# Kernel optimization log

Measured on AMD Instinct MI355X. Metric: run time of the kernel, lower is better.

Reference implementation:

```python
import jax, jax.numpy as jnp
import numpy as np

B = 512          # graphs
M = 200          # nodes per graph
N = B * M        # 102400 total nodes
E = N * 32       # 3,276,800 edges
DIM_IN = 128
K = 30           # SortPool k
F = 32 + 32 + 32 + 1  # concat feature dim = 97


def setup_inputs() -> dict:
    key = jax.random.key(0)
    ks = jax.random.split(key, 20)
    x = jax.random.normal(ks[0], (N, DIM_IN), jnp.float32)
    # within-graph random edges so that batched SortPool is meaningful
    eg = jnp.repeat(jnp.arange(B, dtype=jnp.int32), E // B)  # graph id per edge
    src = eg * M + jax.random.randint(ks[1], (E,), 0, M, dtype=jnp.int32)
    dst = eg * M + jax.random.randint(ks[2], (E,), 0, M, dtype=jnp.int32)
    edge_index = jnp.stack([src, dst])  # [2, E]
    batch = jnp.arange(N, dtype=jnp.int32) // M  # sorted graph assignment

    def lin(k, fi, fo):
        s = 1.0 / np.sqrt(fi)
        return jax.random.uniform(k, (fi, fo), jnp.float32, -s, s)

    inp = {
        "x": x, "edge_index": edge_index, "batch": batch,
        "W1": lin(ks[3], DIM_IN, 32), "b1": jnp.zeros((32,), jnp.float32),
        "W2": lin(ks[4], 32, 32), "b2": jnp.zeros((32,), jnp.float32),
        "W3": lin(ks[5], 32, 32), "b3": jnp.zeros((32,), jnp.float32),
        "W4": lin(ks[6], 32, 1),  "b4": jnp.zeros((1,), jnp.float32),
        "convW1": jax.random.normal(ks[7], (16, 1, 97), jnp.float32) * 0.05,
        "convb1": jnp.zeros((16,), jnp.float32),
        "convW2": jax.random.normal(ks[8], (32, 16, 5), jnp.float32) * 0.05,
        "convb2": jnp.zeros((32,), jnp.float32),
        "linW1": lin(ks[9], 352, 128), "linb1": jnp.zeros((128,), jnp.float32),
        "linW2": lin(ks[10], 128, 1),  "linb2": jnp.zeros((1,), jnp.float32),
    }
    return inp


def _gcn(x, W, b, src, dst, dinv):
    """PyG GCNConv: D^-1/2 (A+I) D^-1/2 X W + b (degrees include self-loops)."""
    xw = x @ W                                   # [N, Fout]
    norm = dinv[src] * dinv[dst]                 # [E]
    agg = jax.ops.segment_sum(xw[src] * norm[:, None], dst, num_segments=N)
    agg = agg + xw * (dinv * dinv)[:, None]      # self-loop term
    return agg + b


def reference(x, edge_index, batch, W1, b1, W2, b2, W3, b3, W4, b4,
              convW1, convb1, convW2, convb2, linW1, linb1, linW2, linb2):
    src, dst = edge_index[0], edge_index[1]
    deg = jax.ops.segment_sum(jnp.ones((E,), x.dtype), dst, num_segments=N) + 1.0
    dinv = jax.lax.rsqrt(deg)

    h1 = jnp.tanh(_gcn(x, W1, b1, src, dst, dinv))
    h2 = jnp.tanh(_gcn(h1, W2, b2, src, dst, dinv))
    h3 = jnp.tanh(_gcn(h2, W3, b3, src, dst, dinv))
    h4 = jnp.tanh(_gcn(h3, W4, b4, src, dst, dinv))
    h = jnp.concatenate([h1, h2, h3, h4], axis=-1)  # [N, 97]

    # SortPool: batch is block-contiguous with M nodes/graph -> dense [B, M, F]
    hd = h.reshape(B, M, F)
    order = jnp.argsort(-hd[:, :, -1], axis=1)[:, :K]          # top-K by last channel
    top = jnp.take_along_axis(hd, order[:, :, None], axis=1)   # [B, K, 97]

    seq = top.reshape(B, 1, K * F)                             # [B, 1, 2910]
    dn = ("NCH", "OIH", "NCH")
    c1 = jax.lax.conv_general_dilated(seq, convW1, (97,), "VALID",
                                      dimension_numbers=dn) + convb1[None, :, None]
    c1 = jax.nn.relu(c1)                                       # [B, 16, 30]
    c1 = c1.reshape(B, 16, 15, 2).max(axis=-1)                 # MaxPool1d(2,2)
    c2 = jax.lax.conv_general_dilated(c1, convW2, (1,), "VALID",
                                      dimension_numbers=dn) + convb2[None, :, None]
    c2 = jax.nn.relu(c2)                                       # [B, 32, 11]

    flat = c2.reshape(B, 352)
    hlin = jax.nn.relu(flat @ linW1 + linb1)                   # dropout = identity (eval)
    out = jax.nn.sigmoid(hlin @ linW2 + linb2)                 # [B, 1]
    return out
```

## Files before the change

### kernel.cpp

```cpp
#include <hip/hip_runtime.h>
#include <hip/hip_fp16.h>


#define TPB   512
#define GRID  512
#define MG    200
#define EPG   6400
#define EE    (512 * EPG)

#define OFF_BUFX 0
#define OFF_HCUR 28944
#define OFF_CSR  57744
#define OFF_ROFF 64944
#define OFF_CNT  65760
#define OFF_CUR  66560
#define OFF_DINV 67360
#define OFF_H4   68160
#define OFF_RANK 68960
#define OFF_ORD  69760
#define OFF_BIAS 69880
#define OFF_RED  70136
#define OFF_WREG 70208
#define OFF_HIST 74560
#define OFF_PERM 74688
#define SMEM_BYTES 75488

#define QPAD 0xC8C8C8C8u

__device__ __forceinline__ float fast_tanh(float x) {
    const float e = __expf(2.0f * x);
    return 1.0f - 2.0f / (e + 1.0f);
}

__global__ __launch_bounds__(TPB)
void dgcnn_kernel(
    const float* __restrict__ x,
    const int*   __restrict__ ei,
    const float* __restrict__ W1, const float* __restrict__ b1,
    const float* __restrict__ W2, const float* __restrict__ b2,
    const float* __restrict__ W3, const float* __restrict__ b3,
    const float* __restrict__ W4, const float* __restrict__ b4,
    const float* __restrict__ cW1, const float* __restrict__ cb1,
    const float* __restrict__ cW2, const float* __restrict__ cb2,
    const float* __restrict__ lW1, const float* __restrict__ lb1,
    const float* __restrict__ lW2, const float* __restrict__ lb2,
    __half* __restrict__ arch,
    float* __restrict__ out)
{
    extern __shared__ unsigned char smem[];
    float* bufX = (float*)(smem + OFF_BUFX);
    float* hcur = (float*)(smem + OFF_HCUR);
    unsigned char* csr = (unsigned char*)(smem + OFF_CSR);
    int*   roff = (int*)(smem + OFF_ROFF);
    int*   cnt  = (int*)(smem + OFF_CNT);
    int*   cur  = (int*)(smem + OFF_CUR);
    float* dinv = (float*)(smem + OFF_DINV);
    float* h4k  = (float*)(smem + OFF_H4);
    int*   rank = (int*)(smem + OFF_RANK);
    int*   ord  = (int*)(smem + OFF_ORD);
    float* bias = (float*)(smem + OFF_BIAS);
    float* red  = (float*)(smem + OFF_RED);
    float* wreg = (float*)(smem + OFF_WREG);
    int*   hist = (int*)(smem + OFF_HIST);
    int*   perm = (int*)(smem + OFF_PERM);

    const int g = blockIdx.x;
    const int t = threadIdx.x;
    const int gbase = g * MG;
    const float* xg   = x + (size_t)gbase * 128;
    const int*   srcp = ei + (size_t)g * EPG;
    const int*   dstp = ei + (size_t)EE + (size_t)g * EPG;

    for (int idx = t; idx < 4096; idx += TPB)
        hcur[(idx & 31) * 132 + (idx >> 5)] = W1[idx];
    for (int idx = t; idx < 1800; idx += TPB)
        ((unsigned*)csr)[idx] = QPAD;
    if (t < 32) bias[t] = b1[t];
    if (t < MG) { cnt[t] = 0; rank[t] = 0; }
    if (t >= 480) hist[t - 480] = 0;
    if (t >= 256 && t < 292) bufX[200 * 36 + (t - 256)] = 0.f;
    __syncthreads();

    const int f32lane = t & 31;
    const int islot   = t >> 5;

    {
        const int4* d4p = (const int4*)dstp;
        for (int e4 = t; e4 < EPG / 4; e4 += TPB) {
            const int4 d4 = d4p[e4];
            atomicAdd(&cnt[d4.x - gbase], 1);
            atomicAdd(&cnt[d4.y - gbase], 1);
            atomicAdd(&cnt[d4.z - gbase], 1);
            atomicAdd(&cnt[d4.w - gbase], 1);
        }
    }
    {
        const int f = f32lane;
        const float* wt = hcur + f * 132;
        const float4* xv = (const float4*)xg;
        #pragma unroll
        for (int j0 = 0; j0 < 12; j0 += 6) {
            const int r0 = islot + 16 * j0;
            float a0 = 0.f, a1 = 0.f, a2 = 0.f, a3 = 0.f, a4 = 0.f, a5 = 0.f;
            #pragma unroll 2
            for (int k4 = 0; k4 < 32; ++k4) {
                const float4 w = *(const float4*)(wt + 4 * k4);
                float4 v;
                v = xv[(r0      ) * 32 + k4]; a0 += v.x*w.x + v.y*w.y + v.z*w.z + v.w*w.w;
                v = xv[(r0 + 16 ) * 32 + k4]; a1 += v.x*w.x + v.y*w.y + v.z*w.z + v.w*w.w;
                v = xv[(r0 + 32 ) * 32 + k4]; a2 += v.x*w.x + v.y*w.y + v.z*w.z + v.w*w.w;
                v = xv[(r0 + 48 ) * 32 + k4]; a3 += v.x*w.x + v.y*w.y + v.z*w.z + v.w*w.w;
                v = xv[(r0 + 64 ) * 32 + k4]; a4 += v.x*w.x + v.y*w.y + v.z*w.z + v.w*w.w;
                v = xv[(r0 + 80 ) * 32 + k4]; a5 += v.x*w.x + v.y*w.y + v.z*w.z + v.w*w.w;
            }
            bufX[(r0      ) * 36 + f] = a0;
            bufX[(r0 + 16 ) * 36 + f] = a1;
            bufX[(r0 + 32 ) * 36 + f] = a2;
            bufX[(r0 + 48 ) * 36 + f] = a3;
            bufX[(r0 + 64 ) * 36 + f] = a4;
            bufX[(r0 + 80 ) * 36 + f] = a5;
        }
        if (islot < 8) {
            const int r = 192 + islot;
            float a0 = 0.f;
            #pragma unroll 2
            for (int k4 = 0; k4 < 32; ++k4) {
                const float4 w = *(const float4*)(wt + 4 * k4);
                const float4 v = xv[r * 32 + k4];
                a0 += v.x*w.x + v.y*w.y + v.z*w.z + v.w*w.w;
            }
            bufX[r * 36 + f] = a0;
        }
    }
    __syncthreads();

    if (t >= 256 && t < 256 + MG) {
        const int i = t - 256;
        const int c = cnt[i];
        dinv[i] = 1.0f / sqrtf((float)(c + 1));
        int qc = (c + 4) >> 2;
        if (qc > 31) qc = 31;
        atomicAdd(&hist[31 - qc], 1);
    }
    if (t < 64) {
        if (t == 0) roff[0] = 0;
        int carry = 0;
        #pragma unroll
        for (int c = 0; c < 4; ++c) {
            const int i = c * 64 + t;
            int v = (i < MG) ? ((cnt[i] + 4) & ~3) : 0;
            #pragma unroll
            for (int off = 1; off < 64; off <<= 1) {
                int u = __shfl_up(v, off);
                if (t >= (int)off) v += u;
            }
            if (i < MG) roff[i + 1] = carry + v;
            carry += __shfl(v, 63);
        }
    }
    __syncthreads();

    if (t < MG) {
        int p = roff[t];
        csr[p] = (unsigned char)t;
        cur[t] = p + 1;
    }
    if (t < 32) {
        const int own = hist[t];
        int v = own;
        #pragma unroll
        for (int off = 1; off < 32; off <<= 1) {
            int u = __shfl_up(v, off);
            if (t >= off) v += u;
        }
        hist[t] = v - own;
    }
    __syncthreads();

    {
        const int4* s4p = (const int4*)srcp;
        const int4* d4p = (const int4*)dstp;
        for (int e4 = t; e4 < EPG / 4; e4 += TPB) {
            const int4 s4 = s4p[e4];
            const int4 d4 = d4p[e4];
            int p;
            p = atomicAdd(&cur[d4.x - gbase], 1); csr[p] = (unsigned char)(s4.x - gbase);
            p = atomicAdd(&cur[d4.y - gbase], 1); csr[p] = (unsigned char)(s4.y - gbase);
            p = atomicAdd(&cur[d4.z - gbase], 1); csr[p] = (unsigned char)(s4.z - gbase);
            p = atomicAdd(&cur[d4.w - gbase], 1); csr[p] = (unsigned char)(s4.w - gbase);
        }
    }
    for (int r = islot; r < MG; r += 16) {
        bufX[r * 36 + f32lane] *= dinv[r];
    }
    if (t < MG) {
        int qc = (cnt[t] + 4) >> 2;
        if (qc > 31) qc = 31;
        const int pos = atomicAdd(&hist[31 - qc], 1);
        perm[pos] = t;
    }
    __syncthreads();

    auto agg_layer = [&](int archOff, int bb) {
        const int f4  = (t & 7) << 2;
        const int dsl = t >> 3;

        auto finish = [&](int d, float a0, float a1, float a2, float a3) {
            const float dv = dinv[d];
            const float o0 = fast_tanh(dv * a0 + bias[bb + f4 + 0]);
            const float o1 = fast_tanh(dv * a1 + bias[bb + f4 + 1]);
            const float o2 = fast_tanh(dv * a2 + bias[bb + f4 + 2]);
            const float o3 = fast_tanh(dv * a3 + bias[bb + f4 + 3]);
            *(float4*)(hcur + d * 36 + f4) = make_float4(o0, o1, o2, o3);
            if (archOff >= 0) {
                const __half2 p01 = __floats2half2_rn(o0, o1);
                const __half2 p23 = __floats2half2_rn(o2, o3);
                __half2* dst = (__half2*)(arch + (size_t)(gbase + d) * 64 + archOff + f4);
                dst[0] = p01;
                dst[1] = p23;
            }
        };

        auto pair_rows = [&](int da, int db) {
            const int p1a = roff[da + 1], p1b = roff[db + 1];
            int pa = roff[da], pb = roff[db];
            const int na = (p1a - pa) >> 2, nb = (p1b - pb) >> 2;
            const int iters = na > nb ? na : nb;
            unsigned qa = *(const unsigned*)(csr + pa);
            unsigned qb = *(const unsigned*)(csr + pb);
            float a0=0.f,a1=0.f,a2=0.f,a3=0.f, c0=0.f,c1=0.f,c2=0.f,c3=0.f;
            for (int i = 0; i < iters; ++i) {
                pa += 4; pb += 4;
                const unsigned qa_n = (pa < p1a) ? *(const unsigned*)(csr + pa) : QPAD;
                const unsigned qb_n = (pb < p1b) ? *(const unsigned*)(csr + pb) : QPAD;
                float4 v;
                v = *(const float4*)(bufX + (qa & 255u) * 36 + f4);         a0+=v.x; a1+=v.y; a2+=v.z; a3+=v.w;
                v = *(const float4*)(bufX + ((qa >> 8) & 255u) * 36 + f4);  a0+=v.x; a1+=v.y; a2+=v.z; a3+=v.w;
                v = *(const float4*)(bufX + ((qa >> 16) & 255u) * 36 + f4); a0+=v.x; a1+=v.y; a2+=v.z; a3+=v.w;
                v = *(const float4*)(bufX + (qa >> 24) * 36 + f4);          a0+=v.x; a1+=v.y; a2+=v.z; a3+=v.w;
                v = *(const float4*)(bufX + (qb & 255u) * 36 + f4);         c0+=v.x; c1+=v.y; c2+=v.z; c3+=v.w;
                v = *(const float4*)(bufX + ((qb >> 8) & 255u) * 36 + f4);  c0+=v.x; c1+=v.y; c2+=v.z; c3+=v.w;
                v = *(const float4*)(bufX + ((qb >> 16) & 255u) * 36 + f4); c0+=v.x; c1+=v.y; c2+=v.z; c3+=v.w;
                v = *(const float4*)(bufX + (qb >> 24) * 36 + f4);          c0+=v.x; c1+=v.y; c2+=v.z; c3+=v.w;
                qa = qa_n; qb = qb_n;
            }
            finish(da, a0, a1, a2, a3);
            finish(db, c0, c1, c2, c3);
        };

        auto one_row = [&](int d) {
            const int p1 = roff[d + 1];
            int p = roff[d];
            const int iters = (p1 - p) >> 2;
            unsigned q = *(const unsigned*)(csr + p);
            float a0=0.f,a1=0.f,a2=0.f,a3=0.f;
            for (int i = 0; i < iters; ++i) {
                p += 4;
                const unsigned q_n = (p < p1) ? *(const unsigned*)(csr + p) : QPAD;
                float4 v;
                v = *(const float4*)(bufX + (q & 255u) * 36 + f4);         a0+=v.x; a1+=v.y; a2+=v.z; a3+=v.w;
                v = *(const float4*)(bufX + ((q >> 8) & 255u) * 36 + f4);  a0+=v.x; a1+=v.y; a2+=v.z; a3+=v.w;
                v = *(const float4*)(bufX + ((q >> 16) & 255u) * 36 + f4); a0+=v.x; a1+=v.y; a2+=v.z; a3+=v.w;
                v = *(const float4*)(bufX + (q >> 24) * 36 + f4);          a0+=v.x; a1+=v.y; a2+=v.z; a3+=v.w;
                q = q_n;
            }
            finish(d, a0, a1, a2, a3);
        };

        pair_rows(perm[2 * dsl], perm[2 * dsl + 1]);
        if (dsl < 8) pair_rows(perm[128 + dsl], perm[192 + dsl]);
        else         one_row(perm[128 + dsl]);
    };

    auto gemm_mid = [&](const float* __restrict__ src) {
        const int f2 = t & 15;
        const int sl = t >> 4;
        const float* wp = wreg + f2 * 68;
        {
            float a0A=0.f,a1A=0.f,a2A=0.f,a3A=0.f,a4A=0.f,a5A=0.f;
            float a0B=0.f,a1B=0.f,a2B=0.f,a3B=0.f,a4B=0.f,a5B=0.f;
            #pragma unroll 2
            for (int k4 = 0; k4 < 8; ++k4) {
                const float4 wA = *(const float4*)(wp + k4 * 8);
                const float4 wB = *(const float4*)(wp + k4 * 8 + 4);
                float4 v;
                v = *(const float4*)(src + (sl       ) * 36 + 4 * k4);
                a0A += v.x*wA.x + v.y*wA.y + v.z*wA.z + v.w*wA.w;
                a0B += v.x*wB.x + v.y*wB.y + v.z*wB.z + v.w*wB.w;
                v = *(const float4*)(src + (sl + 32  ) * 36 + 4 * k4);
                a1A += v.x*wA.x + v.y*wA.y + v.z*wA.z + v.w*wA.w;
                a1B += v.x*wB.x + v.y*wB.y + v.z*wB.z + v.w*wB.w;
                v = *(const float4*)(src + (sl + 64  ) * 36 + 4 * k4);
                a2A += v.x*wA.x + v.y*wA.y + v.z*wA.z + v.w*wA.w;
                a2B += v.x*wB.x + v.y*wB.y + v.z*wB.z + v.w*wB.w;
                v = *(const float4*)(src + (sl + 96  ) * 36 + 4 * k4);
                a3A += v.x*wA.x + v.y*wA.y + v.z*wA.z + v.w*wA.w;
                a3B += v.x*wB.x + v.y*wB.y + v.z*wB.z + v.w*wB.w;
                v = *(const float4*)(src + (sl + 128 ) * 36 + 4 * k4);
                a4A += v.x*wA.x + v.y*wA.y + v.z*wA.z + v.w*wA.w;
                a4B += v.x*wB.x + v.y*wB.y + v.z*wB.z + v.w*wB.w;
                v = *(const float4*)(src + (sl + 160 ) * 36 + 4 * k4);
                a5A += v.x*wA.x + v.y*wA.y + v.z*wA.z + v.w*wA.w;
                a5B += v.x*wB.x + v.y*wB.y + v.z*wB.z + v.w*wB.w;
            }
            const int c0 = 2 * f2;
            *(float2*)(bufX + (sl       ) * 36 + c0) = make_float2(dinv[sl      ] * a0A, dinv[sl      ] * a0B);
            *(float2*)(bufX + (sl + 32  ) * 36 + c0) = make_float2(dinv[sl + 32 ] * a1A, dinv[sl + 32 ] * a1B);
            *(float2*)(bufX + (sl + 64  ) * 36 + c0) = make_float2(dinv[sl + 64 ] * a2A, dinv[sl + 64 ] * a2B);
            *(float2*)(bufX + (sl + 96  ) * 36 + c0) = make_float2(dinv[sl + 96 ] * a3A, dinv[sl + 96 ] * a3B);
            *(float2*)(bufX + (sl + 128 ) * 36 + c0) = make_float2(dinv[sl + 128] * a4A, dinv[sl + 128] * a4B);
            *(float2*)(bufX + (sl + 160 ) * 36 + c0) = make_float2(dinv[sl + 160] * a5A, dinv[sl + 160] * a5B);
        }
        if (sl < 8) {
            const int r = 192 + sl;
            float aA = 0.f, aB = 0.f;
            #pragma unroll 2
            for (int k4 = 0; k4 < 8; ++k4) {
                const float4 wA = *(const float4*)(wp + k4 * 8);
                const float4 wB = *(const float4*)(wp + k4 * 8 + 4);
                const float4 v = *(const float4*)(src + r * 36 + 4 * k4);
                aA += v.x*wA.x + v.y*wA.y + v.z*wA.z + v.w*wA.w;
                aB += v.x*wB.x + v.y*wB.y + v.z*wB.z + v.w*wB.w;
            }
            *(float2*)(bufX + r * 36 + 2 * f2) = make_float2(dinv[r] * aA, dinv[r] * aB);
        }
    };

    auto stage_w_paired = [&](const float* __restrict__ W) {
        for (int idx = t; idx < 1024; idx += TPB) {
            const int k = idx >> 5, f = idx & 31;
            wreg[(f >> 1) * 68 + (k >> 2) * 8 + ((f & 1) << 2) + (k & 3)] = W[idx];
        }
    };

    agg_layer(0, 0);
    stage_w_paired(W2);
    if (t < 32) bias[32 + t] = b2[t];
    __syncthreads();

    gemm_mid(hcur);
    __syncthreads();
    agg_layer(32, 32);
    stage_w_paired(W3);
    if (t < 32) bias[t] = b3[t];
    __syncthreads();

    gemm_mid(hcur);
    __syncthreads();
    agg_layer(-1, 0);
    __syncthreads();

    float* topv = bufX;
    float* cw   = bufX + 3008;

    float* scl = (float*)(smem + OFF_CNT);
    if (t < MG) {
        float a = 0.f;
        #pragma unroll 8
        for (int k = 0; k < 32; ++k) a += hcur[t * 36 + k] * W4[k];
        scl[t] = dinv[t] * a;
    }
    if (t == 200) scl[200] = 0.f;
    if (t >= 256) {
        for (int idx = t - 256; idx < 1552; idx += 256) cw[idx] = cW1[idx];
    } else if (t >= 208 && t < 224) {
        bias[t - 208] = cb1[t - 208];
    } else if (t >= 224 && t < 256) {
        bias[16 + (t - 224)] = cb2[t - 224];
    }
    __syncthreads();
    if (t < MG) {
        const int p0 = roff[t], p1 = roff[t + 1];
        float s = 0.f;
        for (int p = p0; p < p1; p += 4) {
            const unsigned q = *(const unsigned*)(csr + p);
            s += scl[q & 255u] + scl[(q >> 8) & 255u]
               + scl[(q >> 16) & 255u] + scl[q >> 24];
        }
        h4k[t] = fast_tanh(dinv[t] * s + b4[0]);
    }
    if (t >= 256) {
        for (int idx = t - 256; idx < 2560; idx += 256) {
            const int o = idx / 80, r = idx - o * 80;
            cw[1552 + o * 81 + r] = cW2[idx];
        }
    }
    __syncthreads();

    {
        const int i = t & 255;
        const int half = t >> 8;
        if (i < MG) {
            const float vi = h4k[i];
            int r = 0;
            const int j0 = half * 100, j1 = half * 100 + 100;
            for (int j = j0; j < j1; ++j) {
                const float vj = h4k[j];
                r += (vj > vi || (vj == vi && j < i)) ? 1 : 0;
            }
            atomicAdd(&rank[i], r);
        }
    }
    __syncthreads();
    if (t < MG) {
        const int r = rank[t];
        if (r < 30) ord[r] = t;
    }
    __syncthreads();

    for (int idx = t; idx < 2910; idx += TPB) {
        const int kk = idx / 97;
        const int ff = idx - kk * 97;
        const int nd = ord[kk];
        float v;
        if      (ff < 64) v = __half2float(arch[(size_t)(gbase + nd) * 64 + ff]);
        else if (ff < 96) v = hcur[nd * 36 + (ff - 64)];
        else              v = h4k[nd];
        topv[kk * 100 + ff] = v;
    }
    __syncthreads();

    float* c1p2 = hcur;
    float* c1pl = hcur + 480;
    float* flat = hcur + 736;
    float* hlin = hcur + 1088;

    if (t < 480) {
        const int o  = t & 15;
        const int tt = t >> 4;
        float a = bias[o];
        const float* wrow = cw + o * 97;
        const float* trow = topv + tt * 100;
        #pragma unroll 4
        for (int f = 0; f < 97; ++f) a += wrow[f] * trow[f];
        c1p2[o * 30 + tt] = fmaxf(a, 0.f);
    }
    __syncthreads();

    if (t < 240) {
        const int o  = t & 15;
        const int tp = t >> 4;
        c1pl[o * 16 + tp] = fmaxf(c1p2[o * 30 + 2 * tp], c1p2[o * 30 + 2 * tp + 1]);
    }
    __syncthreads();

    if (t < 352) {
        const int o  = t & 31;
        const int tt = t >> 5;
        float a = bias[16 + o];
        const float* w2r = cw + 1552 + o * 81;
        #pragma unroll
        for (int i2 = 0; i2 < 16; ++i2) {
            #pragma unroll
            for (int kk = 0; kk < 5; ++kk)
                a += w2r[i2 * 5 + kk] * c1pl[i2 * 16 + tt + kk];
        }
        flat[o * 11 + tt] = fmaxf(a, 0.f);
    } else if (t >= 352 && t < 480) {
        hlin[t - 352] = lb1[t - 352];
    }
    __syncthreads();

    {
        const int f  = t & 127;
        const int kc = t >> 7;
        float a = 0.f;
        const int k0 = kc * 88;
        #pragma unroll 4
        for (int kk = k0; kk < k0 + 88; ++kk) a += flat[kk] * lW1[kk * 128 + f];
        atomicAdd(&hlin[f], a);
    }
    __syncthreads();

    if (t < 128) {
        float p = fmaxf(hlin[t], 0.f) * lW2[t];
        #pragma unroll
        for (int off = 32; off > 0; off >>= 1) p += __shfl_down(p, off);
        if ((t & 63) == 0) red[t >> 6] = p;
    }
    __syncthreads();
    if (t == 0) {
        const float z = red[0] + red[1] + lb2[0];
        out[g] = 1.f / (1.f + expf(-z));
    }
}

extern "C" void kernel_launch(void* const* d_in, const int* in_sizes, int n_in,
                              void* d_out, int out_size, void* d_ws, size_t ws_size,
                              hipStream_t stream) {
    (void)in_sizes; (void)n_in; (void)out_size; (void)ws_size;
    const float* x   = (const float*)d_in[0];
    const int*   ei  = (const int*)d_in[1];
    const float* W1  = (const float*)d_in[3];  const float* b1  = (const float*)d_in[4];
    const float* W2  = (const float*)d_in[5];  const float* b2  = (const float*)d_in[6];
    const float* W3  = (const float*)d_in[7];  const float* b3  = (const float*)d_in[8];
    const float* W4  = (const float*)d_in[9];  const float* b4  = (const float*)d_in[10];
    const float* cW1 = (const float*)d_in[11]; const float* cb1 = (const float*)d_in[12];
    const float* cW2 = (const float*)d_in[13]; const float* cb2 = (const float*)d_in[14];
    const float* lW1 = (const float*)d_in[15]; const float* lb1 = (const float*)d_in[16];
    const float* lW2 = (const float*)d_in[17]; const float* lb2 = (const float*)d_in[18];
    float* out = (float*)d_out;
    __half* arch = (__half*)d_ws;

    hipFuncSetAttribute((const void*)dgcnn_kernel,
                        hipFuncAttributeMaxDynamicSharedMemorySize, SMEM_BYTES);

    dgcnn_kernel<<<GRID, TPB, SMEM_BYTES, stream>>>(
        x, ei, W1, b1, W2, b2, W3, b3, W4, b4,
        cW1, cb1, cW2, cb2, lW1, lb1, lW2, lb2, arch, out);
}
```

Measured before the change: 237.6 us.

## Mirror node features to global memory so half the waves gather via L1/L2

Each layer's dinv-scaled node features are also written to a per-graph global mirror buffer placed in the workspace. During aggregation, every other group of 64 threads gathers neighbour rows from that mirror through the vector-memory path instead of LDS, spreading gather bandwidth across both LDS and cache. The assignment of the last degree-sorted rows is also reversed, and the two-half atomic rank computation is replaced by a single full-range loop per node. The mirror adds global writes and relies on the workspace being large enough; otherwise the kernel falls back to the old LDS-only path.

```diff
diff --git a/kernel.cpp b/kernel.cpp
--- a/kernel.cpp
+++ b/kernel.cpp
@@ -27,6 +27,8 @@
 
 #define QPAD 0xC8C8C8C8u
 
+#define MIR_STRIDE 6432
+
 __device__ __forceinline__ float fast_tanh(float x) {
     const float e = __expf(2.0f * x);
     return 1.0f - 2.0f / (e + 1.0f);
@@ -45,6 +47,7 @@
     const float* __restrict__ lW1, const float* __restrict__ lb1,
     const float* __restrict__ lW2, const float* __restrict__ lb2,
     __half* __restrict__ arch,
+    float* __restrict__ mir,
     float* __restrict__ out)
 {
     extern __shared__ unsigned char smem[];
@@ -56,7 +59,6 @@
     int*   cur  = (int*)(smem + OFF_CUR);
     float* dinv = (float*)(smem + OFF_DINV);
     float* h4k  = (float*)(smem + OFF_H4);
-    int*   rank = (int*)(smem + OFF_RANK);
     int*   ord  = (int*)(smem + OFF_ORD);
     float* bias = (float*)(smem + OFF_BIAS);
     float* red  = (float*)(smem + OFF_RED);
@@ -71,14 +73,22 @@
     const int*   srcp = ei + (size_t)g * EPG;
     const int*   dstp = ei + (size_t)EE + (size_t)g * EPG;
 
+    float* mir1 = mir ? mir + (size_t)g * MIR_STRIDE : nullptr;
+    float* mir2 = mir ? mir + (size_t)512 * MIR_STRIDE + (size_t)g * MIR_STRIDE : nullptr;
+    float* mir3 = mir ? mir + (size_t)1024 * MIR_STRIDE + (size_t)g * MIR_STRIDE : nullptr;
+
     for (int idx = t; idx < 4096; idx += TPB)
         hcur[(idx & 31) * 132 + (idx >> 5)] = W1[idx];
     for (int idx = t; idx < 1800; idx += TPB)
         ((unsigned*)csr)[idx] = QPAD;
     if (t < 32) bias[t] = b1[t];
-    if (t < MG) { cnt[t] = 0; rank[t] = 0; }
+    if (t < MG) cnt[t] = 0;
     if (t >= 480) hist[t - 480] = 0;
     if (t >= 256 && t < 292) bufX[200 * 36 + (t - 256)] = 0.f;
+    if (mir && t >= 320 && t < 416) {
+        const int ly = (t - 320) >> 5, ff = t & 31;
+        (ly == 0 ? mir1 : ly == 1 ? mir2 : mir3)[200 * 32 + ff] = 0.f;
+    }
     __syncthreads();
 
     const int f32lane = t & 31;
@@ -191,7 +201,9 @@
         }
     }
     for (int r = islot; r < MG; r += 16) {
-        bufX[r * 36 + f32lane] *= dinv[r];
+        const float v = bufX[r * 36 + f32lane] * dinv[r];
+        bufX[r * 36 + f32lane] = v;
+        if (mir) mir1[r * 32 + f32lane] = v;
     }
     if (t < MG) {
         int qc = (cnt[t] + 4) >> 2;
@@ -201,9 +213,10 @@
     }
     __syncthreads();
 
-    auto agg_layer = [&](int archOff, int bb) {
+    auto agg_layer = [&](int archOff, int bb, const float* __restrict__ mirL) {
         const int f4  = (t & 7) << 2;
         const int dsl = t >> 3;
+        const bool gp = (mirL != nullptr) && ((t >> 6) & 1);
 
         auto finish = [&](int d, float a0, float a1, float a2, float a3) {
             const float dv = dinv[d];
@@ -267,12 +280,64 @@
             finish(d, a0, a1, a2, a3);
         };
 
-        pair_rows(perm[2 * dsl], perm[2 * dsl + 1]);
-        if (dsl < 8) pair_rows(perm[128 + dsl], perm[192 + dsl]);
-        else         one_row(perm[128 + dsl]);
+        auto pair_rows_G = [&](int da, int db) {
+            const int p1a = roff[da + 1], p1b = roff[db + 1];
+            int pa = roff[da], pb = roff[db];
+            const int na = (p1a - pa) >> 2, nb = (p1b - pb) >> 2;
+            const int iters = na > nb ? na : nb;
+            unsigned qa = *(const unsigned*)(csr + pa);
+            unsigned qb = *(const unsigned*)(csr + pb);
+            float a0=0.f,a1=0.f,a2=0.f,a3=0.f, c0=0.f,c1=0.f,c2=0.f,c3=0.f;
+            for (int i = 0; i < iters; ++i) {
+                pa += 4; pb += 4;
+                const unsigned qa_n = (pa < p1a) ? *(const unsigned*)(csr + pa) : QPAD;
+                const unsigned qb_n = (pb < p1b) ? *(const unsigned*)(csr + pb) : QPAD;
+                float4 v;
+                v = *(const float4*)(mirL + (qa & 255u) * 32 + f4);         a0+=v.x; a1+=v.y; a2+=v.z; a3+=v.w;
+                v = *(const float4*)(mirL + ((qa >> 8) & 255u) * 32 + f4);  a0+=v.x; a1+=v.y; a2+=v.z; a3+=v.w;
+                v = *(const float4*)(mirL + ((qa >> 16) & 255u) * 32 + f4); a0+=v.x; a1+=v.y; a2+=v.z; a3+=v.w;
+                v = *(const float4*)(mirL + (qa >> 24) * 32 + f4);          a0+=v.x; a1+=v.y; a2+=v.z; a3+=v.w;
+                v = *(const float4*)(mirL + (qb & 255u) * 32 + f4);         c0+=v.x; c1+=v.y; c2+=v.z; c3+=v.w;
+                v = *(const float4*)(mirL + ((qb >> 8) & 255u) * 32 + f4);  c0+=v.x; c1+=v.y; c2+=v.z; c3+=v.w;
+                v = *(const float4*)(mirL + ((qb >> 16) & 255u) * 32 + f4); c0+=v.x; c1+=v.y; c2+=v.z; c3+=v.w;
+                v = *(const float4*)(mirL + (qb >> 24) * 32 + f4);          c0+=v.x; c1+=v.y; c2+=v.z; c3+=v.w;
+                qa = qa_n; qb = qb_n;
+            }
+            finish(da, a0, a1, a2, a3);
+            finish(db, c0, c1, c2, c3);
+        };
+
+        auto one_row_G = [&](int d) {
+            const int p1 = roff[d + 1];
+            int p = roff[d];
+            const int iters = (p1 - p) >> 2;
+            unsigned q = *(const unsigned*)(csr + p);
+            float a0=0.f,a1=0.f,a2=0.f,a3=0.f;
+            for (int i = 0; i < iters; ++i) {
+                p += 4;
+                const unsigned q_n = (p < p1) ? *(const unsigned*)(csr + p) : QPAD;
+                float4 v;
+                v = *(const float4*)(mirL + (q & 255u) * 32 + f4);         a0+=v.x; a1+=v.y; a2+=v.z; a3+=v.w;
+                v = *(const float4*)(mirL + ((q >> 8) & 255u) * 32 + f4);  a0+=v.x; a1+=v.y; a2+=v.z; a3+=v.w;
+                v = *(const float4*)(mirL + ((q >> 16) & 255u) * 32 + f4); a0+=v.x; a1+=v.y; a2+=v.z; a3+=v.w;
+                v = *(const float4*)(mirL + (q >> 24) * 32 + f4);          a0+=v.x; a1+=v.y; a2+=v.z; a3+=v.w;
+                q = q_n;
+            }
+            finish(d, a0, a1, a2, a3);
+        };
+
+        if (gp) {
+            pair_rows_G(perm[2 * dsl], perm[2 * dsl + 1]);
+            if (dsl < 8) pair_rows_G(perm[184 + 7 - dsl], perm[192 + 7 - dsl]);
+            else         one_row_G(perm[191 - dsl]);
+        } else {
+            pair_rows(perm[2 * dsl], perm[2 * dsl + 1]);
+            if (dsl < 8) pair_rows(perm[184 + 7 - dsl], perm[192 + 7 - dsl]);
+            else         one_row(perm[191 - dsl]);
+        }
     };
 
-    auto gemm_mid = [&](const float* __restrict__ src) {
+    auto gemm_mid = [&](const float* __restrict__ src, float* __restrict__ mirW) {
         const int f2 = t & 15;
         const int sl = t >> 4;
         const float* wp = wreg + f2 * 68;
@@ -304,12 +369,26 @@
                 a5B += v.x*wB.x + v.y*wB.y + v.z*wB.z + v.w*wB.w;
             }
             const int c0 = 2 * f2;
-            *(float2*)(bufX + (sl       ) * 36 + c0) = make_float2(dinv[sl      ] * a0A, dinv[sl      ] * a0B);
-            *(float2*)(bufX + (sl + 32  ) * 36 + c0) = make_float2(dinv[sl + 32 ] * a1A, dinv[sl + 32 ] * a1B);
-            *(float2*)(bufX + (sl + 64  ) * 36 + c0) = make_float2(dinv[sl + 64 ] * a2A, dinv[sl + 64 ] * a2B);
-            *(float2*)(bufX + (sl + 96  ) * 36 + c0) = make_float2(dinv[sl + 96 ] * a3A, dinv[sl + 96 ] * a3B);
-            *(float2*)(bufX + (sl + 128 ) * 36 + c0) = make_float2(dinv[sl + 128] * a4A, dinv[sl + 128] * a4B);
-            *(float2*)(bufX + (sl + 160 ) * 36 + c0) = make_float2(dinv[sl + 160] * a5A, dinv[sl + 160] * a5B);
+            float2 r0v = make_float2(dinv[sl      ] * a0A, dinv[sl      ] * a0B);
+            float2 r1v = make_float2(dinv[sl + 32 ] * a1A, dinv[sl + 32 ] * a1B);
+            float2 r2v = make_float2(dinv[sl + 64 ] * a2A, dinv[sl + 64 ] * a2B);
+            float2 r3v = make_float2(dinv[sl + 96 ] * a3A, dinv[sl + 96 ] * a3B);
+            float2 r4v = make_float2(dinv[sl + 128] * a4A, dinv[sl + 128] * a4B);
+            float2 r5v = make_float2(dinv[sl + 160] * a5A, dinv[sl + 160] * a5B);
+            *(float2*)(bufX + (sl       ) * 36 + c0) = r0v;
+            *(float2*)(bufX + (sl + 32  ) * 36 + c0) = r1v;
+            *(float2*)(bufX + (sl + 64  ) * 36 + c0) = r2v;
+            *(float2*)(bufX + (sl + 96  ) * 36 + c0) = r3v;
+            *(float2*)(bufX + (sl + 128 ) * 36 + c0) = r4v;
+            *(float2*)(bufX + (sl + 160 ) * 36 + c0) = r5v;
+            if (mirW) {
+                *(float2*)(mirW + (sl       ) * 32 + c0) = r0v;
+                *(float2*)(mirW + (sl + 32  ) * 32 + c0) = r1v;
+                *(float2*)(mirW + (sl + 64  ) * 32 + c0) = r2v;
+                *(float2*)(mirW + (sl + 96  ) * 32 + c0) = r3v;
+                *(float2*)(mirW + (sl + 128 ) * 32 + c0) = r4v;
+                *(float2*)(mirW + (sl + 160 ) * 32 + c0) = r5v;
+            }
         }
         if (sl < 8) {
             const int r = 192 + sl;
@@ -322,7 +401,9 @@
                 aA += v.x*wA.x + v.y*wA.y + v.z*wA.z + v.w*wA.w;
                 aB += v.x*wB.x + v.y*wB.y + v.z*wB.z + v.w*wB.w;
             }
-            *(float2*)(bufX + r * 36 + 2 * f2) = make_float2(dinv[r] * aA, dinv[r] * aB);
+            float2 rv = make_float2(dinv[r] * aA, dinv[r] * aB);
+            *(float2*)(bufX + r * 36 + 2 * f2) = rv;
+            if (mirW) *(float2*)(mirW + r * 32 + 2 * f2) = rv;
         }
     };
 
@@ -333,21 +414,21 @@
         }
     };
 
-    agg_layer(0, 0);
+    agg_layer(0, 0, mir1);
     stage_w_paired(W2);
     if (t < 32) bias[32 + t] = b2[t];
     __syncthreads();
 
-    gemm_mid(hcur);
-    __syncthreads();
-    agg_layer(32, 32);
+    gemm_mid(hcur, mir2);
+    __syncthreads();
+    agg_layer(32, 32, mir2);
     stage_w_paired(W3);
     if (t < 32) bias[t] = b3[t];
     __syncthreads();
 
-    gemm_mid(hcur);
-    __syncthreads();
-    agg_layer(-1, 0);
+    gemm_mid(hcur, mir3);
+    __syncthreads();
+    agg_layer(-1, 0, mir3);
     __syncthreads();
 
     float* topv = bufX;
@@ -387,23 +468,13 @@
     }
     __syncthreads();
 
-    {
-        const int i = t & 255;
-        const int half = t >> 8;
-        if (i < MG) {
-            const float vi = h4k[i];
-            int r = 0;
-            const int j0 = half * 100, j1 = half * 100 + 100;
-            for (int j = j0; j < j1; ++j) {
-                const float vj = h4k[j];
-                r += (vj > vi || (vj == vi && j < i)) ? 1 : 0;
-            }
-            atomicAdd(&rank[i], r);
-        }
-    }
-    __syncthreads();
     if (t < MG) {
-        const int r = rank[t];
+        const float vi = h4k[t];
+        int r = 0;
+        for (int j = 0; j < MG; ++j) {
+            const float vj = h4k[j];
+            r += (vj > vi || (vj == vi && j < t)) ? 1 : 0;
+        }
         if (r < 30) ord[r] = t;
     }
     __syncthreads();
@@ -488,7 +559,7 @@
 extern "C" void kernel_launch(void* const* d_in, const int* in_sizes, int n_in,
                               void* d_out, int out_size, void* d_ws, size_t ws_size,
                               hipStream_t stream) {
-    (void)in_sizes; (void)n_in; (void)out_size; (void)ws_size;
+    (void)in_sizes; (void)n_in; (void)out_size;
     const float* x   = (const float*)d_in[0];
     const int*   ei  = (const int*)d_in[1];
     const float* W1  = (const float*)d_in[3];  const float* b1  = (const float*)d_in[4];
@@ -500,12 +571,17 @@
     const float* lW1 = (const float*)d_in[15]; const float* lb1 = (const float*)d_in[16];
     const float* lW2 = (const float*)d_in[17]; const float* lb2 = (const float*)d_in[18];
     float* out = (float*)d_out;
+
     __half* arch = (__half*)d_ws;
+    const size_t ARCH_BYTES = (size_t)512 * 200 * 64 * 2;
+    const size_t MIR_BYTES  = (size_t)3 * 512 * MIR_STRIDE * 4;
+    float* mir = (ws_size >= ARCH_BYTES + MIR_BYTES)
+               ? (float*)((char*)d_ws + ARCH_BYTES) : nullptr;
 
     hipFuncSetAttribute((const void*)dgcnn_kernel,
                         hipFuncAttributeMaxDynamicSharedMemorySize, SMEM_BYTES);
 
     dgcnn_kernel<<<GRID, TPB, SMEM_BYTES, stream>>>(
         x, ei, W1, b1, W2, b2, W3, b3, W4, b4,
-        cW1, cb1, cW2, cb2, lW1, lb1, lW2, lb2, arch, out);
+        cW1, cb1, cW2, cb2, lW1, lb1, lW2, lb2, arch, mir, out);
 }
```

Result: slower. 281.6 us (+18.5%).
